# Kernel optimization log

Hardware: AMD Instinct MI355X
Metric: run time of the kernel (lower is better)

Reference implementation:

```python
import jax, jax.numpy as jnp
import numpy as np

B, S, HID, NH, HD, NL = 2, 4096, 1024, 16, 64, 128
N_ITER = 6


def setup_inputs() -> dict:
    key = jax.random.key(0)
    ks = jax.random.split(key, 9)
    s = 0.02
    D = NH * HD
    return {
        "X": jax.random.normal(ks[0], (B, S, HID), jnp.float32),
        "mask": jnp.ones((B, S), jnp.float32),
        "Wq": jax.random.normal(ks[1], (HID, D), jnp.float32) * s,
        "bq": jnp.zeros((D,), jnp.float32),
        "Wk": jax.random.normal(ks[2], (HID, D), jnp.float32) * s,
        "bk": jnp.zeros((D,), jnp.float32),
        "Wv": jax.random.normal(ks[3], (HID, D), jnp.float32) * s,
        "bv": jnp.zeros((D,), jnp.float32),
        "Wo": jax.random.normal(ks[4], (D, HID), jnp.float32) * s,
        "bo": jnp.zeros((HID,), jnp.float32),
    }


def iterative_inv(mat, n_iter=N_ITER):
    # Newton-Schulz style pseudo-inverse iteration (Nystromformer 'original' init)
    I = jnp.eye(mat.shape[-1], dtype=mat.dtype)
    K = mat
    V = K.swapaxes(-1, -2) / jnp.max(jnp.sum(K, axis=-2))
    for _ in range(n_iter):
        KV = K @ V
        V = 0.25 * V @ (13.0 * I - KV @ (15.0 * I - KV @ (7.0 * I - KV)))
    return V


def nystrom_core(Q, K, V, mask):
    # Q,K,V: [B,NH,S,HD], mask: [B,S]
    scale = 1.0 / np.sqrt(np.sqrt(HD))  # 1/d^(1/4) applied to both Q and K
    m = mask[:, None, :, None]
    Q = Q * m * scale
    K = K * m * scale
    seg = S // NL
    # landmarks: mean over contiguous segments -> [B,NH,NL,HD]
    Ql = Q.reshape(B, NH, NL, seg, HD).mean(axis=-2)
    Kl = K.reshape(B, NH, NL, seg, HD).mean(axis=-2)
    k1 = jax.nn.softmax(jnp.einsum('bhsd,bhld->bhsl', Q, Kl), axis=-1)   # [B,NH,S,NL]
    k2 = jax.nn.softmax(jnp.einsum('bhld,bhmd->bhlm', Ql, Kl), axis=-1)  # [B,NH,NL,NL]
    k3 = jax.nn.softmax(
        jnp.einsum('bhld,bhsd->bhls', Ql, K) - 1e9 * (1.0 - mask[:, None, None, :]),
        axis=-1)                                                          # [B,NH,NL,S]
    return k1 @ iterative_inv(k2) @ (k3 @ V)                              # [B,NH,S,HD]


def reference(X, mask, Wq, bq, Wk, bk, Wv, bv, Wo, bo):
    def split(Y):  # [B,S,NH*HD] -> [B,NH,S,HD]
        return Y.reshape(B, S, NH, HD).transpose(0, 2, 1, 3)
    Q = split(X @ Wq + bq)
    K = split(X @ Wk + bk)
    V = split(X @ Wv + bv)
    attn = nystrom_core(Q.astype(jnp.float32), K.astype(jnp.float32),
                        V.astype(jnp.float32), mask.astype(jnp.float32))
    out = attn.transpose(0, 2, 1, 3).reshape(B, S, NH * HD)
    return out @ Wo + bo
```

## Files before the change

### kernel.cpp

```cpp
#include <hip/hip_runtime.h>
#include <math.h>

constexpr int cB = 2, cS = 4096, cHID = 1024, cNH = 16, cHD = 64, cNL = 128, cSEG = 32, cD = 1024, cBH = 32;
constexpr float cSCALE = 0.35355339059327373f;

typedef _Float16 f16x8 __attribute__((ext_vector_type(8)));
typedef float f32x4 __attribute__((ext_vector_type(4)));

__device__ inline void gload_lds16(const void* g, void* l) {
    __builtin_amdgcn_global_load_lds(
        (const __attribute__((address_space(1))) void*)g,
        (__attribute__((address_space(3))) void*)l, 16, 0, 0);
}

__global__ __launch_bounds__(256) void cast_x(const float* __restrict__ X, _Float16* __restrict__ Xh)
{
    int i = (blockIdx.x * 256 + threadIdx.x) * 4;
    float4 v = *reinterpret_cast<const float4*>(X + i);
    union { _Float16 h[4]; ushort4 u; } p;
    p.h[0] = (_Float16)v.x; p.h[1] = (_Float16)v.y; p.h[2] = (_Float16)v.z; p.h[3] = (_Float16)v.w;
    *reinterpret_cast<ushort4*>(Xh + i) = p.u;
}

__global__ __launch_bounds__(256) void wcast_t(
    const float* __restrict__ Wq, const float* __restrict__ Wk,
    const float* __restrict__ Wv, const float* __restrict__ Wo,
    _Float16* __restrict__ WqT, _Float16* __restrict__ WkT,
    _Float16* __restrict__ WvT, _Float16* __restrict__ WoT)
{
    __shared__ float tile[32][33];
    const int wsel = blockIdx.z;
    const float* W = (wsel == 0) ? Wq : (wsel == 1 ? Wk : (wsel == 2 ? Wv : Wo));
    _Float16* WT   = (wsel == 0) ? WqT : (wsel == 1 ? WkT : (wsel == 2 ? WvT : WoT));
    const int n0 = blockIdx.x * 32, k0 = blockIdx.y * 32;
    const int t = threadIdx.x;
    const int r = t >> 3, c = (t & 7) * 4;
    float4 v = *reinterpret_cast<const float4*>(W + (size_t)(k0 + r) * cD + n0 + c);
    tile[r][c] = v.x; tile[r][c + 1] = v.y; tile[r][c + 2] = v.z; tile[r][c + 3] = v.w;
    __syncthreads();
    union { _Float16 h[4]; ushort4 u; } p;
    p.h[0] = (_Float16)tile[c + 0][r]; p.h[1] = (_Float16)tile[c + 1][r];
    p.h[2] = (_Float16)tile[c + 2][r]; p.h[3] = (_Float16)tile[c + 3][r];
    *reinterpret_cast<ushort4*>(WT + (size_t)(n0 + r) * cHID + k0 + c) = p.u;
}

__global__ __launch_bounds__(256) void xm_kernel(
    const float* __restrict__ X, const float* __restrict__ mask,
    float* __restrict__ Xm, float* __restrict__ mbar)
{
    const int bl = blockIdx.x;
    const int b = bl >> 7, l = bl & 127;
    const int c = threadIdx.x * 4;
    float4 a = {0.f, 0.f, 0.f, 0.f};
    float msum = 0.f;
    for (int j = 0; j < cSEG; ++j) {
        float m = mask[b * cS + l * cSEG + j];
        float4 x = *reinterpret_cast<const float4*>(X + ((size_t)(b * cS + l * cSEG + j)) * cHID + c);
        a.x += m * x.x; a.y += m * x.y; a.z += m * x.z; a.w += m * x.w;
        msum += m;
    }
    const float inv = 1.0f / cSEG;
    a.x *= inv; a.y *= inv; a.z *= inv; a.w *= inv;
    *reinterpret_cast<float4*>(Xm + (size_t)bl * cHID + c) = a;
    if (threadIdx.x == 0) mbar[bl] = msum * inv;
}

__global__ __launch_bounds__(256) void qkv_gemm_f16(
    const _Float16* __restrict__ Xh, const float* __restrict__ mask,
    const _Float16* __restrict__ WqT, const _Float16* __restrict__ WkT, const _Float16* __restrict__ WvT,
    const float* __restrict__ bq, const float* __restrict__ bk, const float* __restrict__ bv,
    _Float16* __restrict__ Qh, _Float16* __restrict__ Kh, _Float16* __restrict__ Vh)
{
    __shared__ __align__(16) _Float16 As[128 * 64];
    __shared__ __align__(16) _Float16 Bs[128 * 64];
    const int wsel = blockIdx.z;
    const _Float16* WT = (wsel == 0) ? WqT : (wsel == 1 ? WkT : WvT);
    const float* bias  = (wsel == 0) ? bq  : (wsel == 1 ? bk  : bv);
    _Float16* Y        = (wsel == 0) ? Qh  : (wsel == 1 ? Kh  : Vh);
    const int n0 = blockIdx.x * 128, m0 = blockIdx.y * 128;
    const int t = threadIdx.x;
    const int wave = t >> 6, lane = t & 63;
    const int wm = (wave >> 1) * 64, wn = (wave & 1) * 64;
    const int quad = lane >> 4, l15 = lane & 15;
    const int srow = wave * 8 + (lane >> 3);
    const int scol = (lane & 7) * 8;

    f32x4 acc[4][4];
#pragma unroll
    for (int i = 0; i < 4; ++i)
#pragma unroll
        for (int j = 0; j < 4; ++j) acc[i][j] = (f32x4){0.f, 0.f, 0.f, 0.f};

    for (int k0 = 0; k0 < cHID; k0 += 64) {
        const _Float16* aSrc = Xh + (size_t)(m0 + srow) * cHID + k0 + scol;
        const _Float16* bSrc = WT + (size_t)(n0 + srow) * cHID + k0 + scol;
#pragma unroll
        for (int i = 0; i < 4; ++i) {
            gload_lds16(aSrc + (size_t)(i * 32) * cHID, &As[(wave * 8 + i * 32) * 64]);
            gload_lds16(bSrc + (size_t)(i * 32) * cHID, &Bs[(wave * 8 + i * 32) * 64]);
        }
        __syncthreads();
        f16x8 af[2][4], bf[2][4];
#pragma unroll
        for (int kh = 0; kh < 2; ++kh) {
#pragma unroll
            for (int mt = 0; mt < 4; ++mt)
                af[kh][mt] = *reinterpret_cast<const f16x8*>(&As[(wm + mt * 16 + l15) * 64 + kh * 32 + quad * 8]);
#pragma unroll
            for (int nt = 0; nt < 4; ++nt)
                bf[kh][nt] = *reinterpret_cast<const f16x8*>(&Bs[(wn + nt * 16 + l15) * 64 + kh * 32 + quad * 8]);
        }
#pragma unroll
        for (int kh = 0; kh < 2; ++kh)
#pragma unroll
            for (int mt = 0; mt < 4; ++mt)
#pragma unroll
                for (int nt = 0; nt < 4; ++nt)
                    acc[mt][nt] = __builtin_amdgcn_mfma_f32_16x16x32_f16(af[kh][mt], bf[kh][nt], acc[mt][nt], 0, 0, 0);
        __syncthreads();
    }
#pragma unroll
    for (int mt = 0; mt < 4; ++mt) {
#pragma unroll
        for (int r = 0; r < 4; ++r) {
            int R = m0 + wm + mt * 16 + quad * 4 + r;
            int b = R >> 12, s = R & (cS - 1);
            float msc = (wsel < 2) ? mask[b * cS + s] * cSCALE : 1.0f;
#pragma unroll
            for (int nt = 0; nt < 4; ++nt) {
                int Cc = n0 + wn + nt * 16 + l15;
                int h = Cc >> 6, d = Cc & 63;
                float val = (acc[mt][nt][r] + bias[Cc]) * msc;
                Y[((size_t)(b * cNH + h) * cS + s) * cHD + d] = (_Float16)val;
            }
        }
    }
}

__global__ __launch_bounds__(256) void out_gemm_f16(
    const _Float16* __restrict__ Ah, const _Float16* __restrict__ WT,
    const float* __restrict__ bias, float* __restrict__ Y)
{
    __shared__ __align__(16) _Float16 As[128 * 64];
    __shared__ __align__(16) _Float16 Bs[128 * 64];
    const int n0 = blockIdx.x * 128, m0 = blockIdx.y * 128;
    const int t = threadIdx.x;
    const int wave = t >> 6, lane = t & 63;
    const int wm = (wave >> 1) * 64, wn = (wave & 1) * 64;
    const int quad = lane >> 4, l15 = lane & 15;
    const int srow = wave * 8 + (lane >> 3);
    const int scol = (lane & 7) * 8;

    f32x4 acc[4][4];
#pragma unroll
    for (int i = 0; i < 4; ++i)
#pragma unroll
        for (int j = 0; j < 4; ++j) acc[i][j] = (f32x4){0.f, 0.f, 0.f, 0.f};

    for (int k0 = 0; k0 < cD; k0 += 64) {
        const _Float16* aSrc = Ah + (size_t)(m0 + srow) * cD + k0 + scol;
        const _Float16* bSrc = WT + (size_t)(n0 + srow) * cD + k0 + scol;
#pragma unroll
        for (int i = 0; i < 4; ++i) {
            gload_lds16(aSrc + (size_t)(i * 32) * cD, &As[(wave * 8 + i * 32) * 64]);
            gload_lds16(bSrc + (size_t)(i * 32) * cD, &Bs[(wave * 8 + i * 32) * 64]);
        }
        __syncthreads();
        f16x8 af[2][4], bf[2][4];
#pragma unroll
        for (int kh = 0; kh < 2; ++kh) {
#pragma unroll
            for (int mt = 0; mt < 4; ++mt)
                af[kh][mt] = *reinterpret_cast<const f16x8*>(&As[(wm + mt * 16 + l15) * 64 + kh * 32 + quad * 8]);
#pragma unroll
            for (int nt = 0; nt < 4; ++nt)
                bf[kh][nt] = *reinterpret_cast<const f16x8*>(&Bs[(wn + nt * 16 + l15) * 64 + kh * 32 + quad * 8]);
        }
#pragma unroll
        for (int kh = 0; kh < 2; ++kh)
#pragma unroll
            for (int mt = 0; mt < 4; ++mt)
#pragma unroll
                for (int nt = 0; nt < 4; ++nt)
                    acc[mt][nt] = __builtin_amdgcn_mfma_f32_16x16x32_f16(af[kh][mt], bf[kh][nt], acc[mt][nt], 0, 0, 0);
        __syncthreads();
    }
#pragma unroll
    for (int mt = 0; mt < 4; ++mt) {
#pragma unroll
        for (int r = 0; r < 4; ++r) {
            int R = m0 + wm + mt * 16 + quad * 4 + r;
#pragma unroll
            for (int nt = 0; nt < 4; ++nt) {
                int Cc = n0 + wn + nt * 16 + l15;
                Y[(size_t)R * cHID + Cc] = acc[mt][nt][r] + bias[Cc];
            }
        }
    }
}

__global__ __launch_bounds__(256) void lgemm(
    const float* __restrict__ Xm, const float* __restrict__ mbar,
    const float* __restrict__ Wq, const float* __restrict__ bq,
    const float* __restrict__ Wk, const float* __restrict__ bk,
    float* __restrict__ Ql, float* __restrict__ Kl,
    _Float16* __restrict__ Qlh, _Float16* __restrict__ Klh)
{
    __shared__ __align__(16) float As[16][68];
    __shared__ __align__(16) float Bs[16][68];
    const int tid = threadIdx.x;
    const int wsel = blockIdx.z;
    const float* W    = wsel ? Wk : Wq;
    const float* bias = wsel ? bk : bq;
    float* Yl         = wsel ? Kl : Ql;
    _Float16* Ylh     = wsel ? Klh : Qlh;
    const int c0 = blockIdx.x * 64, r0 = blockIdx.y * 64;
    const int tx = tid & 15, ty = tid >> 4;
    const int am = tid >> 2, ak = (tid & 3) * 4;
    const int bkk = tid >> 4, bn = (tid & 15) * 4;

    float acc[4][4] = {};
    for (int k0 = 0; k0 < cHID; k0 += 16) {
        float4 a4 = *reinterpret_cast<const float4*>(Xm + (size_t)(r0 + am) * cHID + k0 + ak);
        As[ak + 0][am] = a4.x; As[ak + 1][am] = a4.y; As[ak + 2][am] = a4.z; As[ak + 3][am] = a4.w;
        float4 b4 = *reinterpret_cast<const float4*>(W + (size_t)(k0 + bkk) * cD + c0 + bn);
        *reinterpret_cast<float4*>(&Bs[bkk][bn]) = b4;
        __syncthreads();
#pragma unroll
        for (int kk = 0; kk < 16; ++kk) {
            float4 av  = *reinterpret_cast<const float4*>(&As[kk][ty * 4]);
            float4 bv4 = *reinterpret_cast<const float4*>(&Bs[kk][tx * 4]);
            float a_[4] = {av.x, av.y, av.z, av.w};
            float b_[4] = {bv4.x, bv4.y, bv4.z, bv4.w};
#pragma unroll
            for (int i = 0; i < 4; ++i)
#pragma unroll
                for (int j = 0; j < 4; ++j) acc[i][j] += a_[i] * b_[j];
        }
        __syncthreads();
    }
#pragma unroll
    for (int i = 0; i < 4; ++i) {
        int r = r0 + ty * 4 + i;
        int b = r >> 7, l = r & 127;
        float mb = mbar[r];
#pragma unroll
        for (int j = 0; j < 4; ++j) {
            int c = c0 + tx * 4 + j;
            int h = c >> 6, d = c & 63;
            float val = (acc[i][j] + mb * bias[c]) * cSCALE;
            size_t idx = ((size_t)(b * cNH + h) * cNL + l) * cHD + d;
            Yl[idx] = val;
            Ylh[idx] = (_Float16)val;
        }
    }
}

__global__ __launch_bounds__(128) void k2_softmax(
    const float* __restrict__ Ql, const float* __restrict__ Kl, float* __restrict__ k2)
{
    __shared__ __align__(16) float qrow[64];
    __shared__ float red[128];
    int bh = blockIdx.x >> 7, i = blockIdx.x & 127;
    int j = threadIdx.x;
    if (j < 64) qrow[j] = Ql[(bh * cNL + i) * cHD + j];
    __syncthreads();
    const float4* q4  = reinterpret_cast<const float4*>(qrow);
    const float4* kl4 = reinterpret_cast<const float4*>(Kl + (bh * cNL + j) * cHD);
    float dot = 0.f;
#pragma unroll
    for (int u = 0; u < 16; ++u) {
        float4 a = q4[u], b = kl4[u];
        dot += a.x * b.x + a.y * b.y + a.z * b.z + a.w * b.w;
    }
    red[j] = dot; __syncthreads();
    for (int off = 64; off > 0; off >>= 1) { if (j < off) red[j] = fmaxf(red[j], red[j + off]); __syncthreads(); }
    float m = red[0]; __syncthreads();
    float e = expf(dot - m);
    red[j] = e; __syncthreads();
    for (int off = 64; off > 0; off >>= 1) { if (j < off) red[j] += red[j + off]; __syncthreads(); }
    k2[(bh * cNL + i) * cNL + j] = e / red[0];
}

__global__ __launch_bounds__(128) void colsum_max(const float* __restrict__ k2, int* __restrict__ cmax)
{
    __shared__ float red[128];
    int bh = blockIdx.x, j = threadIdx.x;
    float s = 0.f;
    for (int i = 0; i < cNL; ++i) s += k2[(bh * cNL + i) * cNL + j];
    red[j] = s; __syncthreads();
    for (int off = 64; off > 0; off >>= 1) { if (j < off) red[j] = fmaxf(red[j], red[j + off]); __syncthreads(); }
    if (j == 0) atomicMax(cmax, __float_as_int(red[0]));
}

__device__ inline void split2(float v, _Float16& h, _Float16& l) {
    h = (_Float16)v;
    l = (_Float16)(v - (float)h);
}

#define NYS_MFMA(a, b, c) __builtin_amdgcn_mfma_f32_16x16x32_f16((a), (b), (c), 0, 0, 0)

#define NYS_PRODUCT(PH, PL, LH, LL)                                                     \
    {                                                                                   \
        _Pragma("unroll")                                                               \
        for (int nt_ = 0; nt_ < 4; ++nt_) {                                             \
            f32x4 a0_ = (f32x4){0.f, 0.f, 0.f, 0.f};                                    \
            f32x4 a1_ = (f32x4){0.f, 0.f, 0.f, 0.f};                                    \
            _Pragma("unroll")                                                           \
            for (int k0_ = 0; k0_ < 4; ++k0_) {                                         \
                const int boff_ = (wcb + nt_ * 16) * 136 + k0_ * 32 + quad * 8;         \
                f16x8 bh_ = *reinterpret_cast<const f16x8*>(&PH[boff_]);                \
                f16x8 bl_ = *reinterpret_cast<const f16x8*>(&PL[boff_]);                \
                a0_ = NYS_MFMA(LH[0][k0_], bh_, a0_);                                   \
                a1_ = NYS_MFMA(LH[1][k0_], bh_, a1_);                                   \
                a0_ = NYS_MFMA(LL[0][k0_], bh_, a0_);                                   \
                a1_ = NYS_MFMA(LL[1][k0_], bh_, a1_);                                   \
                a0_ = NYS_MFMA(LH[0][k0_], bl_, a0_);                                   \
                a1_ = NYS_MFMA(LH[1][k0_], bl_, a1_);                                   \
            }                                                                           \
            acc[0][nt_] = a0_; acc[1][nt_] = a1_;                                       \
        }                                                                               \
    }

#define NYS_SCATTER_W(alphav)                                                           \
    {                                                                                   \
        _Pragma("unroll")                                                               \
        for (int mt_ = 0; mt_ < 2; ++mt_) {                                             \
            _Pragma("unroll")                                                           \
            for (int nt_ = 0; nt_ < 4; ++nt_) {                                         \
                int col_ = wcb + nt_ * 16;                                              \
                int rb_  = wr * 32 + mt_ * 16 + quad * 4;                               \
                ushort4 ph_, pl_;                                                       \
                _Pragma("unroll")                                                       \
                for (int r_ = 0; r_ < 4; ++r_) {                                        \
                    float v_ = ((rb_ + r_) == col_ ? (alphav) : 0.f) - acc[mt_][nt_][r_]; \
                    _Float16 h_, l_; split2(v_, h_, l_);                                \
                    ((unsigned short*)&ph_)[r_] = __builtin_bit_cast(unsigned short, h_); \
                    ((unsigned short*)&pl_)[r_] = __builtin_bit_cast(unsigned short, l_); \
                }                                                                       \
                *reinterpret_cast<ushort4*>(&Whi_s[col_ * 136 + rb_]) = ph_;            \
                *reinterpret_cast<ushort4*>(&Wlo_s[col_ * 136 + rb_]) = pl_;            \
            }                                                                           \
        }                                                                               \
    }

__global__ __launch_bounds__(512, 2) void nys_fused(
    const float* __restrict__ k2, const int* __restrict__ cmax, float* __restrict__ V6)
{
    __shared__ __align__(16) _Float16 Vhi_s[128 * 136];
    __shared__ __align__(16) _Float16 Vlo_s[128 * 136];
    __shared__ __align__(16) _Float16 Whi_s[128 * 136];
    __shared__ __align__(16) _Float16 Wlo_s[128 * 136];
    const int bh = blockIdx.x;
    const int t = threadIdx.x;
    const int wave = t >> 6, lane = t & 63;
    const int wr = wave >> 1, wc = wave & 1;
    const int quad = lane >> 4, l15 = lane & 15;
    const int wcb = wc * 64 + l15;
    const float* Kg = k2 + (size_t)bh * (cNL * cNL);
    const float invc = 1.0f / __int_as_float(*cmax);

#pragma unroll
    for (int i = 0; i < 8; ++i) {
        int idx = t + i * 512;
        int row = idx >> 5, c4 = (idx & 31) * 4;
        float4 v = *reinterpret_cast<const float4*>(Kg + (size_t)row * cNL + c4);
        ushort4 ph, pl;
        _Float16 h, l;
        split2(v.x * invc, h, l); ((unsigned short*)&ph)[0] = __builtin_bit_cast(unsigned short, h); ((unsigned short*)&pl)[0] = __builtin_bit_cast(unsigned short, l);
        split2(v.y * invc, h, l); ((unsigned short*)&ph)[1] = __builtin_bit_cast(unsigned short, h); ((unsigned short*)&pl)[1] = __builtin_bit_cast(unsigned short, l);
        split2(v.z * invc, h, l); ((unsigned short*)&ph)[2] = __builtin_bit_cast(unsigned short, h); ((unsigned short*)&pl)[2] = __builtin_bit_cast(unsigned short, l);
        split2(v.w * invc, h, l); ((unsigned short*)&ph)[3] = __builtin_bit_cast(unsigned short, h); ((unsigned short*)&pl)[3] = __builtin_bit_cast(unsigned short, l);
        *reinterpret_cast<ushort4*>(&Vhi_s[row * 136 + c4]) = ph;
        *reinterpret_cast<ushort4*>(&Vlo_s[row * 136 + c4]) = pl;
    }

    f16x8 Khi[2][4], Klo[2][4];
#pragma unroll
    for (int mt = 0; mt < 2; ++mt) {
        const int rowL = wr * 32 + mt * 16 + l15;
#pragma unroll
        for (int k0 = 0; k0 < 4; ++k0) {
            const float* src = Kg + (size_t)rowL * cNL + k0 * 32 + quad * 8;
            float4 v0 = *reinterpret_cast<const float4*>(src);
            float4 v1 = *reinterpret_cast<const float4*>(src + 4);
            union { f16x8 v; _Float16 e[8]; } hh, ll;
            split2(v0.x, hh.e[0], ll.e[0]); split2(v0.y, hh.e[1], ll.e[1]);
            split2(v0.z, hh.e[2], ll.e[2]); split2(v0.w, hh.e[3], ll.e[3]);
            split2(v1.x, hh.e[4], ll.e[4]); split2(v1.y, hh.e[5], ll.e[5]);
            split2(v1.z, hh.e[6], ll.e[6]); split2(v1.w, hh.e[7], ll.e[7]);
            Khi[mt][k0] = hh.v; Klo[mt][k0] = ll.v;
        }
    }
    __syncthreads();

    f32x4 acc[2][4];
    f16x8 Ahi[2][4], Alo[2][4];

    for (int it = 0; it < 6; ++it) {
        NYS_PRODUCT(Vhi_s, Vlo_s, Khi, Klo);
        NYS_SCATTER_W(7.0f);
        __syncthreads();

#pragma unroll
        for (int mt = 0; mt < 2; ++mt) {
            const int rowL = wr * 32 + mt * 16 + l15;
#pragma unroll
            for (int k0 = 0; k0 < 4; ++k0) {
                union { f16x8 v; _Float16 e[8]; } hh, ll;
#pragma unroll
                for (int j = 0; j < 8; ++j) {
                    int kk = k0 * 32 + quad * 8 + j;
                    float s = (float)Whi_s[kk * 136 + rowL] + (float)Wlo_s[kk * 136 + rowL];
                    float a = ((kk == rowL) ? 7.0f : 0.0f) - s;
                    split2(a, hh.e[j], ll.e[j]);
                }
                Ahi[mt][k0] = hh.v; Alo[mt][k0] = ll.v;
            }
        }

        NYS_PRODUCT(Whi_s, Wlo_s, Ahi, Alo);
        __syncthreads();
        NYS_SCATTER_W(15.0f);
        __syncthreads();

        NYS_PRODUCT(Whi_s, Wlo_s, Ahi, Alo);
        __syncthreads();
        NYS_SCATTER_W(13.0f);
        __syncthreads();

#pragma unroll
        for (int mt = 0; mt < 2; ++mt)
#pragma unroll
            for (int nt = 0; nt < 4; ++nt) acc[mt][nt] = (f32x4){0.f, 0.f, 0.f, 0.f};
#pragma unroll
        for (int k0 = 0; k0 < 4; ++k0) {
            f16x8 Vlh[2], Vll[2];
#pragma unroll
            for (int mt = 0; mt < 2; ++mt) {
                const int rowL = wr * 32 + mt * 16 + l15;
                union { f16x8 v; _Float16 e[8]; } hh, ll;
#pragma unroll
                for (int j = 0; j < 8; ++j) {
                    int kk = k0 * 32 + quad * 8 + j;
                    hh.e[j] = Vhi_s[kk * 136 + rowL];
                    ll.e[j] = Vlo_s[kk * 136 + rowL];
                }
                Vlh[mt] = hh.v; Vll[mt] = ll.v;
            }
#pragma unroll
            for (int nt = 0; nt < 4; ++nt) {
                const int boff = (wcb + nt * 16) * 136 + k0 * 32 + quad * 8;
                f16x8 bh_ = *reinterpret_cast<const f16x8*>(&Whi_s[boff]);
                f16x8 bl_ = *reinterpret_cast<const f16x8*>(&Wlo_s[boff]);
                acc[0][nt] = NYS_MFMA(Vlh[0], bh_, acc[0][nt]);
                acc[1][nt] = NYS_MFMA(Vlh[1], bh_, acc[1][nt]);
                acc[0][nt] = NYS_MFMA(Vll[0], bh_, acc[0][nt]);
                acc[1][nt] = NYS_MFMA(Vll[1], bh_, acc[1][nt]);
                acc[0][nt] = NYS_MFMA(Vlh[0], bl_, acc[0][nt]);
                acc[1][nt] = NYS_MFMA(Vlh[1], bl_, acc[1][nt]);
            }
        }
        if (it < 5) {
            __syncthreads();
#pragma unroll
            for (int mt = 0; mt < 2; ++mt) {
#pragma unroll
                for (int nt = 0; nt < 4; ++nt) {
                    int col = wcb + nt * 16;
                    int rb  = wr * 32 + mt * 16 + quad * 4;
                    ushort4 ph, pl;
#pragma unroll
                    for (int r = 0; r < 4; ++r) {
                        _Float16 h, l; split2(0.25f * acc[mt][nt][r], h, l);
                        ((unsigned short*)&ph)[r] = __builtin_bit_cast(unsigned short, h);
                        ((unsigned short*)&pl)[r] = __builtin_bit_cast(unsigned short, l);
                    }
                    *reinterpret_cast<ushort4*>(&Vhi_s[col * 136 + rb]) = ph;
                    *reinterpret_cast<ushort4*>(&Vlo_s[col * 136 + rb]) = pl;
                }
            }
            __syncthreads();
        }
    }
#pragma unroll
    for (int mt = 0; mt < 2; ++mt)
#pragma unroll
        for (int nt = 0; nt < 4; ++nt)
#pragma unroll
            for (int r = 0; r < 4; ++r) {
                int row = wr * 32 + mt * 16 + quad * 4 + r;
                int col = wcb + nt * 16;
                V6[(size_t)bh * (cNL * cNL) + row * cNL + col] = 0.25f * acc[mt][nt][r];
            }
}

__global__ __launch_bounds__(256) void vtrans(const _Float16* __restrict__ Vh, _Float16* __restrict__ VTh)
{
    __shared__ ushort T[64][72];
    const int s0 = blockIdx.x * 64, bh = blockIdx.y;
    const int t = threadIdx.x;
    const _Float16* vb = Vh + ((size_t)bh * cS + s0) * cHD;
#pragma unroll
    for (int i = 0; i < 2; ++i) {
        int idx = t + i * 256;
        int row = idx >> 3, c8 = idx & 7;
        f16x8 v = *reinterpret_cast<const f16x8*>(vb + (size_t)row * cHD + c8 * 8);
#pragma unroll
        for (int j = 0; j < 8; ++j) T[row][c8 * 8 + j] = ((ushort*)&v)[j];
    }
    __syncthreads();
    _Float16* vt = VTh + (size_t)bh * cHD * cS;
#pragma unroll
    for (int i = 0; i < 2; ++i) {
        int idx = t + i * 256;
        int d = idx >> 3, s8 = idx & 7;
        f16x8 o;
#pragma unroll
        for (int j = 0; j < 8; ++j) ((ushort*)&o)[j] = T[s8 * 8 + j][d];
        *reinterpret_cast<f16x8*>(vt + (size_t)d * cS + s0 + s8 * 8) = o;
    }
}

__global__ __launch_bounds__(256) void k3v_mfma(
    const _Float16* __restrict__ Qlh, const _Float16* __restrict__ Kh,
    const _Float16* __restrict__ VTh, const float* __restrict__ mask,
    float* __restrict__ Opart, float* __restrict__ mpart, float* __restrict__ spart)
{
    __shared__ __align__(16) _Float16 Ps[128 * 72];
    __shared__ float msk[256];
    const int z = blockIdx.x, bh = blockIdx.y;
    const int b = bh >> 4;
    const int sbase = z * 256;
    const int t = threadIdx.x;
    const int wave = t >> 6, lane = t & 63;
    const int quad = lane >> 4, l15 = lane & 15;

    msk[t] = mask[b * cS + sbase + t];

    f16x8 aq[2][2];
    const _Float16* qlg = Qlh + (size_t)bh * cNL * cHD;
#pragma unroll
    for (int mt = 0; mt < 2; ++mt)
#pragma unroll
        for (int k0 = 0; k0 < 2; ++k0)
            aq[mt][k0] = *reinterpret_cast<const f16x8*>(
                qlg + (size_t)(wave * 32 + mt * 16 + l15) * cHD + k0 * 32 + quad * 8);

    float mrun[2][4], srun[2][4];
    f32x4 accO[2][4];
#pragma unroll
    for (int mt = 0; mt < 2; ++mt)
#pragma unroll
        for (int r = 0; r < 4; ++r) { mrun[mt][r] = -1e30f; srun[mt][r] = 0.f; }
#pragma unroll
    for (int mt = 0; mt < 2; ++mt)
#pragma unroll
        for (int dt = 0; dt < 4; ++dt) accO[mt][dt] = (f32x4){0.f, 0.f, 0.f, 0.f};

    __syncthreads();

    const _Float16* kg = Kh + (size_t)bh * cS * cHD;
    const _Float16* vg = VTh + (size_t)bh * cHD * cS;

    for (int step = 0; step < 4; ++step) {
        const int st = sbase + step * 64;
        f32x4 accS[2][4];
#pragma unroll
        for (int mt = 0; mt < 2; ++mt)
#pragma unroll
            for (int nt = 0; nt < 4; ++nt) accS[mt][nt] = (f32x4){0.f, 0.f, 0.f, 0.f};
#pragma unroll
        for (int k0 = 0; k0 < 2; ++k0)
#pragma unroll
            for (int nt = 0; nt < 4; ++nt) {
                f16x8 bk = *reinterpret_cast<const f16x8*>(
                    kg + (size_t)(st + nt * 16 + l15) * cHD + k0 * 32 + quad * 8);
#pragma unroll
                for (int mt = 0; mt < 2; ++mt)
                    accS[mt][nt] = __builtin_amdgcn_mfma_f32_16x16x32_f16(aq[mt][k0], bk, accS[mt][nt], 0, 0, 0);
            }
#pragma unroll
        for (int nt = 0; nt < 4; ++nt) {
            float pen = 1e9f * (1.0f - msk[step * 64 + nt * 16 + l15]);
#pragma unroll
            for (int mt = 0; mt < 2; ++mt)
#pragma unroll
                for (int r = 0; r < 4; ++r) accS[mt][nt][r] -= pen;
        }
#pragma unroll
        for (int mt = 0; mt < 2; ++mt) {
#pragma unroll
            for (int r = 0; r < 4; ++r) {
                float tmax = fmaxf(fmaxf(accS[mt][0][r], accS[mt][1][r]),
                                   fmaxf(accS[mt][2][r], accS[mt][3][r]));
#pragma unroll
                for (int w = 1; w < 16; w <<= 1) tmax = fmaxf(tmax, __shfl_xor(tmax, w, 16));
                float mnew = fmaxf(mrun[mt][r], tmax);
                float alpha = __expf(mrun[mt][r] - mnew);
                float ts = 0.f;
#pragma unroll
                for (int nt = 0; nt < 4; ++nt) {
                    float e = __expf(accS[mt][nt][r] - mnew);
                    accS[mt][nt][r] = e; ts += e;
                }
#pragma unroll
                for (int w = 1; w < 16; w <<= 1) ts += __shfl_xor(ts, w, 16);
                srun[mt][r] = srun[mt][r] * alpha + ts;
                mrun[mt][r] = mnew;
#pragma unroll
                for (int dt = 0; dt < 4; ++dt) accO[mt][dt][r] *= alpha;
            }
        }
#pragma unroll
        for (int mt = 0; mt < 2; ++mt)
#pragma unroll
            for (int nt = 0; nt < 4; ++nt)
#pragma unroll
                for (int r = 0; r < 4; ++r)
                    Ps[(wave * 32 + mt * 16 + quad * 4 + r) * 72 + nt * 16 + l15] =
                        (_Float16)accS[mt][nt][r];
#pragma unroll
        for (int k0 = 0; k0 < 2; ++k0) {
            f16x8 ap[2];
#pragma unroll
            for (int mt = 0; mt < 2; ++mt)
                ap[mt] = *reinterpret_cast<const f16x8*>(
                    &Ps[(wave * 32 + mt * 16 + l15) * 72 + k0 * 32 + quad * 8]);
#pragma unroll
            for (int dt = 0; dt < 4; ++dt) {
                f16x8 bv = *reinterpret_cast<const f16x8*>(
                    vg + (size_t)(dt * 16 + l15) * cS + st + k0 * 32 + quad * 8);
#pragma unroll
                for (int mt = 0; mt < 2; ++mt)
                    accO[mt][dt] = __builtin_amdgcn_mfma_f32_16x16x32_f16(ap[mt], bv, accO[mt][dt], 0, 0, 0);
            }
        }
    }
    const int rowbase = bh * cNL + wave * 32;
#pragma unroll
    for (int mt = 0; mt < 2; ++mt)
#pragma unroll
        for (int dt = 0; dt < 4; ++dt)
#pragma unroll
            for (int r = 0; r < 4; ++r)
                Opart[(size_t)(z * 4096 + rowbase + mt * 16 + quad * 4 + r) * cHD + dt * 16 + l15] =
                    accO[mt][dt][r];
    if (l15 == 0) {
#pragma unroll
        for (int mt = 0; mt < 2; ++mt)
#pragma unroll
            for (int r = 0; r < 4; ++r) {
                int prow = z * 4096 + rowbase + mt * 16 + quad * 4 + r;
                mpart[prow] = mrun[mt][r];
                spart[prow] = srun[mt][r];
            }
    }
}

__global__ __launch_bounds__(256) void k3v_reduce(
    const float* __restrict__ Opart, const float* __restrict__ mpart,
    const float* __restrict__ spart, float* __restrict__ CV)
{
    const int t = threadIdx.x;
    const int row = blockIdx.x * 4 + (t >> 6);
    const int d = t & 63;
    float mstar = -1e30f;
#pragma unroll
    for (int z = 0; z < 16; ++z) mstar = fmaxf(mstar, mpart[z * 4096 + row]);
    float ssum = 0.f, acc = 0.f;
#pragma unroll
    for (int z = 0; z < 16; ++z) {
        float w = __expf(mpart[z * 4096 + row] - mstar);
        ssum += w * spart[z * 4096 + row];
        acc  += w * Opart[(size_t)(z * 4096 + row) * cHD + d];
    }
    CV[(size_t)row * cHD + d] = acc / ssum;
}

__global__ __launch_bounds__(256) void w2_matmul(
    const float* __restrict__ V6, const float* __restrict__ CV, _Float16* __restrict__ W2T)
{
    __shared__ __align__(16) float CVs[128][64];
    const int bh = blockIdx.x, t = threadIdx.x;
    for (int k = 0; k < 32; ++k) { int idx = t + k * 256; CVs[idx >> 6][idx & 63] = CV[bh * 8192 + idx]; }
    __syncthreads();
    const int tx = t & 15, ty = t >> 4;
    float acc[8][4] = {};
    for (int k = 0; k < 128; ++k) {
        float4 b4 = *reinterpret_cast<const float4*>(&CVs[k][tx * 4]);
#pragma unroll
        for (int i = 0; i < 8; ++i) {
            float a = V6[(bh * cNL + ty * 8 + i) * cNL + k];
            acc[i][0] += a * b4.x; acc[i][1] += a * b4.y; acc[i][2] += a * b4.z; acc[i][3] += a * b4.w;
        }
    }
    _Float16* wt = W2T + (size_t)bh * cHD * cNL;
#pragma unroll
    for (int i = 0; i < 8; ++i)
#pragma unroll
        for (int j = 0; j < 4; ++j)
            wt[(size_t)(tx * 4 + j) * cNL + ty * 8 + i] = (_Float16)acc[i][j];
}

__global__ __launch_bounds__(256) void k1_mfma(
    const _Float16* __restrict__ Qh, const _Float16* __restrict__ Klh,
    const _Float16* __restrict__ W2T, _Float16* __restrict__ ctxh)
{
    __shared__ __align__(16) _Float16 Qs[64 * 72];
    __shared__ __align__(16) _Float16 Ps[64 * 136];
    const int s0 = blockIdx.x * 64, bh = blockIdx.y;
    const int b = bh >> 4, h = bh & 15;
    const int t = threadIdx.x;
    const int wave = t >> 6, lane = t & 63;
    const int quad = lane >> 4, l15 = lane & 15;

    {
        const _Float16* qg = Qh + ((size_t)bh * cS + s0) * cHD;
#pragma unroll
        for (int i = 0; i < 2; ++i) {
            int idx = t + i * 256;
            int row = idx >> 3, c8 = idx & 7;
            *reinterpret_cast<f16x8*>(&Qs[row * 72 + c8 * 8]) =
                *reinterpret_cast<const f16x8*>(qg + (size_t)row * cHD + c8 * 8);
        }
    }
    __syncthreads();

    const _Float16* klg = Klh + (size_t)bh * cNL * cHD;
    f32x4 accS[8];
#pragma unroll
    for (int nt = 0; nt < 8; ++nt) accS[nt] = (f32x4){0.f, 0.f, 0.f, 0.f};
#pragma unroll
    for (int k0 = 0; k0 < 2; ++k0) {
        f16x8 aq = *reinterpret_cast<const f16x8*>(&Qs[(wave * 16 + l15) * 72 + k0 * 32 + quad * 8]);
#pragma unroll
        for (int nt = 0; nt < 8; ++nt) {
            f16x8 bk = *reinterpret_cast<const f16x8*>(klg + (size_t)(nt * 16 + l15) * cHD + k0 * 32 + quad * 8);
            accS[nt] = __builtin_amdgcn_mfma_f32_16x16x32_f16(aq, bk, accS[nt], 0, 0, 0);
        }
    }

    float rmax[4] = {-1e30f, -1e30f, -1e30f, -1e30f};
#pragma unroll
    for (int nt = 0; nt < 8; ++nt)
#pragma unroll
        for (int r = 0; r < 4; ++r) rmax[r] = fmaxf(rmax[r], accS[nt][r]);
#pragma unroll
    for (int r = 0; r < 4; ++r)
#pragma unroll
        for (int w = 1; w < 16; w <<= 1) rmax[r] = fmaxf(rmax[r], __shfl_xor(rmax[r], w, 16));
    float rsum[4] = {0.f, 0.f, 0.f, 0.f};
#pragma unroll
    for (int nt = 0; nt < 8; ++nt)
#pragma unroll
        for (int r = 0; r < 4; ++r) { accS[nt][r] = __expf(accS[nt][r] - rmax[r]); rsum[r] += accS[nt][r]; }
#pragma unroll
    for (int r = 0; r < 4; ++r) {
#pragma unroll
        for (int w = 1; w < 16; w <<= 1) rsum[r] += __shfl_xor(rsum[r], w, 16);
        rsum[r] = 1.0f / rsum[r];
    }
#pragma unroll
    for (int nt = 0; nt < 8; ++nt)
#pragma unroll
        for (int r = 0; r < 4; ++r)
            Ps[(wave * 16 + quad * 4 + r) * 136 + nt * 16 + l15] = (_Float16)(accS[nt][r] * rsum[r]);
    __syncthreads();

    const _Float16* wtg = W2T + (size_t)bh * cHD * cNL;
    f32x4 accO[4];
#pragma unroll
    for (int nt = 0; nt < 4; ++nt) accO[nt] = (f32x4){0.f, 0.f, 0.f, 0.f};
#pragma unroll
    for (int k0 = 0; k0 < 4; ++k0) {
        f16x8 ap = *reinterpret_cast<const f16x8*>(&Ps[(wave * 16 + l15) * 136 + k0 * 32 + quad * 8]);
#pragma unroll
        for (int nt = 0; nt < 4; ++nt) {
            f16x8 bw = *reinterpret_cast<const f16x8*>(wtg + (size_t)(nt * 16 + l15) * cNL + k0 * 32 + quad * 8);
            accO[nt] = __builtin_amdgcn_mfma_f32_16x16x32_f16(ap, bw, accO[nt], 0, 0, 0);
        }
    }
#pragma unroll
    for (int nt = 0; nt < 4; ++nt)
#pragma unroll
        for (int r = 0; r < 4; ++r) {
            int s = s0 + wave * 16 + quad * 4 + r;
            int d = nt * 16 + l15;
            ctxh[((size_t)(b * cS) + s) * cD + h * cHD + d] = (_Float16)accO[nt][r];
        }
}

extern "C" void kernel_launch(void* const* d_in, const int* in_sizes, int n_in,
                              void* d_out, int out_size, void* d_ws, size_t ws_size,
                              hipStream_t stream)
{
    const float* X    = (const float*)d_in[0];
    const float* mask = (const float*)d_in[1];
    const float* Wq   = (const float*)d_in[2];
    const float* bq   = (const float*)d_in[3];
    const float* Wk   = (const float*)d_in[4];
    const float* bk   = (const float*)d_in[5];
    const float* Wv   = (const float*)d_in[6];
    const float* bv   = (const float*)d_in[7];
    const float* Wo   = (const float*)d_in[8];
    const float* bo   = (const float*)d_in[9];
    float* out = (float*)d_out;

    float* ws = (float*)d_ws;
    size_t off = 0;
    const size_t szQKV = (size_t)cBH * cS * cHD;
    const size_t szL   = (size_t)cBH * cNL * cHD;
    const size_t szM   = (size_t)cBH * cNL * cNL;
    float* Qr   = ws + off; off += szQKV;
    float* Kr   = ws + off; off += szQKV;
    float* Vr   = ws + off; off += szQKV;
    _Float16* Xh  = (_Float16*)(ws + off); off += szQKV / 2;
    _Float16* WqT = (_Float16*)(ws + off); off += 524288;
    _Float16* WkT = (_Float16*)(ws + off); off += 524288;
    _Float16* WvT = (_Float16*)(ws + off); off += 524288;
    _Float16* WoT = (_Float16*)(ws + off); off += 524288;
    float* Xm   = ws + off; off += (size_t)cB * cNL * cHID;
    float* mbar = ws + off; off += 256;
    float* Ql  = ws + off; off += szL;
    float* Kl  = ws + off; off += szL;
    float* k2  = ws + off; off += szM;
    float* Vb0 = ws + off; off += szM;
    float* Vb1 = ws + off; off += szM;
    float* Zb  = ws + off; off += szM;
    float* T2b = ws + off; off += szM;
    float* T3b = ws + off; off += szM;
    float* CV  = ws + off; off += szL;
    _Float16* Qlh  = (_Float16*)(ws + off); off += szL / 2;
    _Float16* Klh  = (_Float16*)(ws + off); off += szL / 2;
    _Float16* W2Th = (_Float16*)(ws + off); off += szL / 2;
    int*   cmax = (int*)(ws + off); off += 16;
    float* mpart = ws + off; off += 65536;
    float* spart = ws + off; off += 65536;

    _Float16* Qh   = (_Float16*)Qr;
    float*    Opart = Qr + szQKV / 2;
    _Float16* Kh   = (_Float16*)Kr;
    _Float16* ctxh = (_Float16*)(Kr + szQKV / 2);
    _Float16* Vh   = (_Float16*)Vr;
    _Float16* VTh  = (_Float16*)(Vr + szQKV / 2);

    (void)Vb1; (void)Zb; (void)T2b; (void)T3b;

    hipMemsetAsync(cmax, 0, sizeof(int), stream);

    cast_x<<<(int)(szQKV / 1024), 256, 0, stream>>>(X, Xh);
    wcast_t<<<dim3(32, 32, 4), 256, 0, stream>>>(Wq, Wk, Wv, Wo, WqT, WkT, WvT, WoT);
    xm_kernel<<<cB * cNL, 256, 0, stream>>>(X, mask, Xm, mbar);

    qkv_gemm_f16<<<dim3(cD / 128, (cB * cS) / 128, 3), 256, 0, stream>>>(
        Xh, mask, WqT, WkT, WvT, bq, bk, bv, Qh, Kh, Vh);
    vtrans<<<dim3(cS / 64, cBH), 256, 0, stream>>>(Vh, VTh);
    lgemm<<<dim3(cD / 64, (cB * cNL) / 64, 2), 256, 0, stream>>>(Xm, mbar, Wq, bq, Wk, bk, Ql, Kl, Qlh, Klh);

    k2_softmax<<<cBH * cNL, 128, 0, stream>>>(Ql, Kl, k2);
    colsum_max<<<cBH, 128, 0, stream>>>(k2, cmax);

    nys_fused<<<cBH, 512, 0, stream>>>(k2, cmax, Vb0);

    k3v_mfma<<<dim3(16, cBH), 256, 0, stream>>>(Qlh, Kh, VTh, mask, Opart, mpart, spart);
    k3v_reduce<<<1024, 256, 0, stream>>>(Opart, mpart, spart, CV);
    w2_matmul<<<cBH, 256, 0, stream>>>(Vb0, CV, W2Th);
    k1_mfma<<<dim3(cS / 64, cBH), 256, 0, stream>>>(Qh, Klh, W2Th, ctxh);
    out_gemm_f16<<<dim3(cHID / 128, (cB * cS) / 128), 256, 0, stream>>>(ctxh, WoT, bo, out);
}
```

Measured before the change: 544.3 us.

## Reformulate Newton-Schulz inverse iteration around symmetric K·K^T products

Rewrites the Nyström pseudo-inverse kernel so each iteration works on A = c·K·K^T and a polynomial in it, instead of forming K·V and chaining products with V. The product of per-iteration factors M is accumulated in global ping-pong buffers, and the final multiply by K^T and the 1/c scale move into w2_matmul. The goal is fewer dependent 128x128 matmul stages and LDS transposes per iteration. The cost is extra global traffic for M, a second matmul in w2_matmul, and numerical behaviour that depends on the algebraic identity and on hi/lo fp16 splitting.

```diff
diff --git a/kernel.cpp b/kernel.cpp
--- a/kernel.cpp
+++ b/kernel.cpp
@@ -297,8 +297,22 @@
     h = (_Float16)v;
     l = (_Float16)(v - (float)h);
 }
+__device__ inline unsigned short f16bits(_Float16 h) { return __builtin_bit_cast(unsigned short, h); }
 
 #define NYS_MFMA(a, b, c) __builtin_amdgcn_mfma_f32_16x16x32_f16((a), (b), (c), 0, 0, 0)
+
+#define NYS_PRELOAD(PH, PL, LH, LL)                                                     \
+    {                                                                                   \
+        _Pragma("unroll")                                                               \
+        for (int mt_ = 0; mt_ < 2; ++mt_) {                                             \
+            const int rowL_ = wr * 32 + mt_ * 16 + l15;                                 \
+            _Pragma("unroll")                                                           \
+            for (int k0_ = 0; k0_ < 4; ++k0_) {                                         \
+                LH[mt_][k0_] = *reinterpret_cast<const f16x8*>(&PH[rowL_ * 136 + k0_ * 32 + quad * 8]); \
+                LL[mt_][k0_] = *reinterpret_cast<const f16x8*>(&PL[rowL_ * 136 + k0_ * 32 + quad * 8]); \
+            }                                                                           \
+        }                                                                               \
+    }
 
 #define NYS_PRODUCT(PH, PL, LH, LL)                                                     \
     {                                                                                   \
@@ -322,33 +336,12 @@
         }                                                                               \
     }
 
-#define NYS_SCATTER_W(alphav)                                                           \
-    {                                                                                   \
-        _Pragma("unroll")                                                               \
-        for (int mt_ = 0; mt_ < 2; ++mt_) {                                             \
-            _Pragma("unroll")                                                           \
-            for (int nt_ = 0; nt_ < 4; ++nt_) {                                         \
-                int col_ = wcb + nt_ * 16;                                              \
-                int rb_  = wr * 32 + mt_ * 16 + quad * 4;                               \
-                ushort4 ph_, pl_;                                                       \
-                _Pragma("unroll")                                                       \
-                for (int r_ = 0; r_ < 4; ++r_) {                                        \
-                    float v_ = ((rb_ + r_) == col_ ? (alphav) : 0.f) - acc[mt_][nt_][r_]; \
-                    _Float16 h_, l_; split2(v_, h_, l_);                                \
-                    ((unsigned short*)&ph_)[r_] = __builtin_bit_cast(unsigned short, h_); \
-                    ((unsigned short*)&pl_)[r_] = __builtin_bit_cast(unsigned short, l_); \
-                }                                                                       \
-                *reinterpret_cast<ushort4*>(&Whi_s[col_ * 136 + rb_]) = ph_;            \
-                *reinterpret_cast<ushort4*>(&Wlo_s[col_ * 136 + rb_]) = pl_;            \
-            }                                                                           \
-        }                                                                               \
-    }
-
 __global__ __launch_bounds__(512, 2) void nys_fused(
-    const float* __restrict__ k2, const int* __restrict__ cmax, float* __restrict__ V6)
-{
-    __shared__ __align__(16) _Float16 Vhi_s[128 * 136];
-    __shared__ __align__(16) _Float16 Vlo_s[128 * 136];
+    const float* __restrict__ k2, const int* __restrict__ cmax,
+    float* __restrict__ Mg0, float* __restrict__ Mg1)
+{
+    __shared__ __align__(16) _Float16 Ahi_s[128 * 136];
+    __shared__ __align__(16) _Float16 Alo_s[128 * 136];
     __shared__ __align__(16) _Float16 Whi_s[128 * 136];
     __shared__ __align__(16) _Float16 Wlo_s[128 * 136];
     const int bh = blockIdx.x;
@@ -357,142 +350,153 @@
     const int wr = wave >> 1, wc = wave & 1;
     const int quad = lane >> 4, l15 = lane & 15;
     const int wcb = wc * 64 + l15;
-    const float* Kg = k2 + (size_t)bh * (cNL * cNL);
-    const float invc = 1.0f / __int_as_float(*cmax);
-
-#pragma unroll
-    for (int i = 0; i < 8; ++i) {
-        int idx = t + i * 512;
-        int row = idx >> 5, c4 = (idx & 31) * 4;
-        float4 v = *reinterpret_cast<const float4*>(Kg + (size_t)row * cNL + c4);
-        ushort4 ph, pl;
-        _Float16 h, l;
-        split2(v.x * invc, h, l); ((unsigned short*)&ph)[0] = __builtin_bit_cast(unsigned short, h); ((unsigned short*)&pl)[0] = __builtin_bit_cast(unsigned short, l);
-        split2(v.y * invc, h, l); ((unsigned short*)&ph)[1] = __builtin_bit_cast(unsigned short, h); ((unsigned short*)&pl)[1] = __builtin_bit_cast(unsigned short, l);
-        split2(v.z * invc, h, l); ((unsigned short*)&ph)[2] = __builtin_bit_cast(unsigned short, h); ((unsigned short*)&pl)[2] = __builtin_bit_cast(unsigned short, l);
-        split2(v.w * invc, h, l); ((unsigned short*)&ph)[3] = __builtin_bit_cast(unsigned short, h); ((unsigned short*)&pl)[3] = __builtin_bit_cast(unsigned short, l);
-        *reinterpret_cast<ushort4*>(&Vhi_s[row * 136 + c4]) = ph;
-        *reinterpret_cast<ushort4*>(&Vlo_s[row * 136 + c4]) = pl;
-    }
-
-    f16x8 Khi[2][4], Klo[2][4];
-#pragma unroll
-    for (int mt = 0; mt < 2; ++mt) {
-        const int rowL = wr * 32 + mt * 16 + l15;
-#pragma unroll
-        for (int k0 = 0; k0 < 4; ++k0) {
-            const float* src = Kg + (size_t)rowL * cNL + k0 * 32 + quad * 8;
-            float4 v0 = *reinterpret_cast<const float4*>(src);
-            float4 v1 = *reinterpret_cast<const float4*>(src + 4);
-            union { f16x8 v; _Float16 e[8]; } hh, ll;
-            split2(v0.x, hh.e[0], ll.e[0]); split2(v0.y, hh.e[1], ll.e[1]);
-            split2(v0.z, hh.e[2], ll.e[2]); split2(v0.w, hh.e[3], ll.e[3]);
-            split2(v1.x, hh.e[4], ll.e[4]); split2(v1.y, hh.e[5], ll.e[5]);
-            split2(v1.z, hh.e[6], ll.e[6]); split2(v1.w, hh.e[7], ll.e[7]);
-            Khi[mt][k0] = hh.v; Klo[mt][k0] = ll.v;
+    const float* Kg = k2 + (size_t)bh * 16384;
+    float* Mg0b = Mg0 + (size_t)bh * 16384;
+    float* Mg1b = Mg1 + (size_t)bh * 16384;
+    const float sc = sqrtf(1.0f / __int_as_float(*cmax));
+
+    {
+        const int row = t >> 2, c0 = (t & 3) * 32;
+        const float* src = Kg + row * 128 + c0;
+        _Float16* dh = &Whi_s[row * 136 + c0];
+        _Float16* dl = &Wlo_s[row * 136 + c0];
+#pragma unroll
+        for (int u = 0; u < 32; u += 4) {
+            float4 v = *reinterpret_cast<const float4*>(src + u);
+            ushort4 ph, pl; _Float16 h, l;
+            split2(v.x * sc, h, l); ph.x = f16bits(h); pl.x = f16bits(l);
+            split2(v.y * sc, h, l); ph.y = f16bits(h); pl.y = f16bits(l);
+            split2(v.z * sc, h, l); ph.z = f16bits(h); pl.z = f16bits(l);
+            split2(v.w * sc, h, l); ph.w = f16bits(h); pl.w = f16bits(l);
+            *reinterpret_cast<ushort4*>(dh + u) = ph;
+            *reinterpret_cast<ushort4*>(dl + u) = pl;
         }
     }
     __syncthreads();
 
     f32x4 acc[2][4];
-    f16x8 Ahi[2][4], Alo[2][4];
+    f16x8 Fh[2][4], Fl[2][4];
+
+    NYS_PRELOAD(Whi_s, Wlo_s, Fh, Fl);
+    NYS_PRODUCT(Whi_s, Wlo_s, Fh, Fl);
+#pragma unroll
+    for (int mt = 0; mt < 2; ++mt)
+#pragma unroll
+        for (int nt = 0; nt < 4; ++nt) {
+            const int col = wcb + nt * 16;
+            const int rb  = wr * 32 + mt * 16 + quad * 4;
+            ushort4 ph, pl;
+#pragma unroll
+            for (int r = 0; r < 4; ++r) {
+                _Float16 h, l; split2(acc[mt][nt][r], h, l);
+                ((unsigned short*)&ph)[r] = f16bits(h);
+                ((unsigned short*)&pl)[r] = f16bits(l);
+            }
+            *reinterpret_cast<ushort4*>(&Ahi_s[col * 136 + rb]) = ph;
+            *reinterpret_cast<ushort4*>(&Alo_s[col * 136 + rb]) = pl;
+        }
+    __syncthreads();
 
     for (int it = 0; it < 6; ++it) {
-        NYS_PRODUCT(Vhi_s, Vlo_s, Khi, Klo);
-        NYS_SCATTER_W(7.0f);
-        __syncthreads();
-
-#pragma unroll
-        for (int mt = 0; mt < 2; ++mt) {
-            const int rowL = wr * 32 + mt * 16 + l15;
-#pragma unroll
-            for (int k0 = 0; k0 < 4; ++k0) {
-                union { f16x8 v; _Float16 e[8]; } hh, ll;
-#pragma unroll
-                for (int j = 0; j < 8; ++j) {
-                    int kk = k0 * 32 + quad * 8 + j;
-                    float s = (float)Whi_s[kk * 136 + rowL] + (float)Wlo_s[kk * 136 + rowL];
-                    float a = ((kk == rowL) ? 7.0f : 0.0f) - s;
-                    split2(a, hh.e[j], ll.e[j]);
+        NYS_PRELOAD(Ahi_s, Alo_s, Fh, Fl);
+        NYS_PRODUCT(Ahi_s, Alo_s, Fh, Fl);
+#pragma unroll
+        for (int mt = 0; mt < 2; ++mt)
+#pragma unroll
+            for (int nt = 0; nt < 4; ++nt) {
+                const int col = wcb + nt * 16;
+                const int rb  = wr * 32 + mt * 16 + quad * 4;
+                ushort4 ah = *reinterpret_cast<const ushort4*>(&Ahi_s[col * 136 + rb]);
+                ushort4 al = *reinterpret_cast<const ushort4*>(&Alo_s[col * 136 + rb]);
+                ushort4 ph, pl;
+#pragma unroll
+                for (int r = 0; r < 4; ++r) {
+                    float av = (float)__builtin_bit_cast(_Float16, ((unsigned short*)&ah)[r])
+                             + (float)__builtin_bit_cast(_Float16, ((unsigned short*)&al)[r]);
+                    float v = ((rb + r) == col ? 15.0f : 0.0f) - 7.0f * av + acc[mt][nt][r];
+                    _Float16 h, l; split2(v, h, l);
+                    ((unsigned short*)&ph)[r] = f16bits(h);
+                    ((unsigned short*)&pl)[r] = f16bits(l);
                 }
-                Ahi[mt][k0] = hh.v; Alo[mt][k0] = ll.v;
-            }
-        }
-
-        NYS_PRODUCT(Whi_s, Wlo_s, Ahi, Alo);
-        __syncthreads();
-        NYS_SCATTER_W(15.0f);
-        __syncthreads();
-
-        NYS_PRODUCT(Whi_s, Wlo_s, Ahi, Alo);
-        __syncthreads();
-        NYS_SCATTER_W(13.0f);
-        __syncthreads();
-
+                *reinterpret_cast<ushort4*>(&Whi_s[col * 136 + rb]) = ph;
+                *reinterpret_cast<ushort4*>(&Wlo_s[col * 136 + rb]) = pl;
+            }
+        __syncthreads();
+        NYS_PRODUCT(Whi_s, Wlo_s, Fh, Fl);
+        __syncthreads();
 #pragma unroll
         for (int mt = 0; mt < 2; ++mt)
 #pragma unroll
-            for (int nt = 0; nt < 4; ++nt) acc[mt][nt] = (f32x4){0.f, 0.f, 0.f, 0.f};
-#pragma unroll
-        for (int k0 = 0; k0 < 4; ++k0) {
-            f16x8 Vlh[2], Vll[2];
+            for (int nt = 0; nt < 4; ++nt) {
+                const int col = wcb + nt * 16;
+                const int rb  = wr * 32 + mt * 16 + quad * 4;
+                ushort4 ph, pl; float4 mv;
+#pragma unroll
+                for (int r = 0; r < 4; ++r) {
+                    float v = ((rb + r) == col ? 13.0f : 0.0f) - acc[mt][nt][r];
+                    _Float16 h, l; split2(v, h, l);
+                    ((unsigned short*)&ph)[r] = f16bits(h);
+                    ((unsigned short*)&pl)[r] = f16bits(l);
+                    ((float*)&mv)[r] = 0.25f * v;
+                }
+                *reinterpret_cast<ushort4*>(&Whi_s[col * 136 + rb]) = ph;
+                *reinterpret_cast<ushort4*>(&Wlo_s[col * 136 + rb]) = pl;
+                if (it == 0)
+                    *reinterpret_cast<float4*>(&Mg0b[col * 128 + rb]) = mv;
+            }
+        __syncthreads();
+        NYS_PRODUCT(Whi_s, Wlo_s, Fh, Fl);
+#pragma unroll
+        for (int mt = 0; mt < 2; ++mt)
+#pragma unroll
+            for (int nt = 0; nt < 4; ++nt) {
+                const int col = wcb + nt * 16;
+                const int rb  = wr * 32 + mt * 16 + quad * 4;
+                ushort4 ph, pl;
+#pragma unroll
+                for (int r = 0; r < 4; ++r) {
+                    _Float16 h, l; split2(0.25f * acc[mt][nt][r], h, l);
+                    ((unsigned short*)&ph)[r] = f16bits(h);
+                    ((unsigned short*)&pl)[r] = f16bits(l);
+                }
+                *reinterpret_cast<ushort4*>(&Ahi_s[col * 136 + rb]) = ph;
+                *reinterpret_cast<ushort4*>(&Alo_s[col * 136 + rb]) = pl;
+            }
+        if (it >= 1) {
+            const float* Mr = (it & 1) ? Mg0b : Mg1b;
+            float*       Mw = (it & 1) ? Mg1b : Mg0b;
+            f16x8 Mh[2][4], Ml[2][4];
 #pragma unroll
             for (int mt = 0; mt < 2; ++mt) {
                 const int rowL = wr * 32 + mt * 16 + l15;
-                union { f16x8 v; _Float16 e[8]; } hh, ll;
-#pragma unroll
-                for (int j = 0; j < 8; ++j) {
-                    int kk = k0 * 32 + quad * 8 + j;
-                    hh.e[j] = Vhi_s[kk * 136 + rowL];
-                    ll.e[j] = Vlo_s[kk * 136 + rowL];
+#pragma unroll
+                for (int k0 = 0; k0 < 4; ++k0) {
+                    const float* src = Mr + rowL * 128 + k0 * 32 + quad * 8;
+                    float4 v0 = *reinterpret_cast<const float4*>(src);
+                    float4 v1 = *reinterpret_cast<const float4*>(src + 4);
+                    union { f16x8 v; _Float16 e[8]; } hh, ll;
+                    split2(v0.x, hh.e[0], ll.e[0]); split2(v0.y, hh.e[1], ll.e[1]);
+                    split2(v0.z, hh.e[2], ll.e[2]); split2(v0.w, hh.e[3], ll.e[3]);
+                    split2(v1.x, hh.e[4], ll.e[4]); split2(v1.y, hh.e[5], ll.e[5]);
+                    split2(v1.z, hh.e[6], ll.e[6]); split2(v1.w, hh.e[7], ll.e[7]);
+                    Mh[mt][k0] = hh.v; Ml[mt][k0] = ll.v;
                 }
-                Vlh[mt] = hh.v; Vll[mt] = ll.v;
-            }
-#pragma unroll
-            for (int nt = 0; nt < 4; ++nt) {
-                const int boff = (wcb + nt * 16) * 136 + k0 * 32 + quad * 8;
-                f16x8 bh_ = *reinterpret_cast<const f16x8*>(&Whi_s[boff]);
-                f16x8 bl_ = *reinterpret_cast<const f16x8*>(&Wlo_s[boff]);
-                acc[0][nt] = NYS_MFMA(Vlh[0], bh_, acc[0][nt]);
-                acc[1][nt] = NYS_MFMA(Vlh[1], bh_, acc[1][nt]);
-                acc[0][nt] = NYS_MFMA(Vll[0], bh_, acc[0][nt]);
-                acc[1][nt] = NYS_MFMA(Vll[1], bh_, acc[1][nt]);
-                acc[0][nt] = NYS_MFMA(Vlh[0], bl_, acc[0][nt]);
-                acc[1][nt] = NYS_MFMA(Vlh[1], bl_, acc[1][nt]);
-            }
-        }
-        if (it < 5) {
-            __syncthreads();
-#pragma unroll
-            for (int mt = 0; mt < 2; ++mt) {
+            }
+            NYS_PRODUCT(Whi_s, Wlo_s, Mh, Ml);
+#pragma unroll
+            for (int mt = 0; mt < 2; ++mt)
 #pragma unroll
                 for (int nt = 0; nt < 4; ++nt) {
-                    int col = wcb + nt * 16;
-                    int rb  = wr * 32 + mt * 16 + quad * 4;
-                    ushort4 ph, pl;
-#pragma unroll
-                    for (int r = 0; r < 4; ++r) {
-                        _Float16 h, l; split2(0.25f * acc[mt][nt][r], h, l);
-                        ((unsigned short*)&ph)[r] = __builtin_bit_cast(unsigned short, h);
-                        ((unsigned short*)&pl)[r] = __builtin_bit_cast(unsigned short, l);
-                    }
-                    *reinterpret_cast<ushort4*>(&Vhi_s[col * 136 + rb]) = ph;
-                    *reinterpret_cast<ushort4*>(&Vlo_s[col * 136 + rb]) = pl;
+                    const int col = wcb + nt * 16;
+                    const int rb  = wr * 32 + mt * 16 + quad * 4;
+                    float4 mv;
+#pragma unroll
+                    for (int r = 0; r < 4; ++r) ((float*)&mv)[r] = 0.25f * acc[mt][nt][r];
+                    *reinterpret_cast<float4*>(&Mw[col * 128 + rb]) = mv;
                 }
-            }
-            __syncthreads();
-        }
-    }
-#pragma unroll
-    for (int mt = 0; mt < 2; ++mt)
-#pragma unroll
-        for (int nt = 0; nt < 4; ++nt)
-#pragma unroll
-            for (int r = 0; r < 4; ++r) {
-                int row = wr * 32 + mt * 16 + quad * 4 + r;
-                int col = wcb + nt * 16;
-                V6[(size_t)bh * (cNL * cNL) + row * cNL + col] = 0.25f * acc[mt][nt][r];
-            }
+        }
+        __syncthreads();
+    }
 }
 
 __global__ __launch_bounds__(256) void vtrans(const _Float16* __restrict__ Vh, _Float16* __restrict__ VTh)
@@ -679,28 +683,51 @@
 }
 
 __global__ __launch_bounds__(256) void w2_matmul(
-    const float* __restrict__ V6, const float* __restrict__ CV, _Float16* __restrict__ W2T)
-{
-    __shared__ __align__(16) float CVs[128][64];
+    const float* __restrict__ k2, const float* __restrict__ M6,
+    const int* __restrict__ cmax, const float* __restrict__ CV,
+    _Float16* __restrict__ W2T)
+{
+    __shared__ __align__(16) float CVs[128][68];
+    __shared__ __align__(16) float Us[128][68];
     const int bh = blockIdx.x, t = threadIdx.x;
-    for (int k = 0; k < 32; ++k) { int idx = t + k * 256; CVs[idx >> 6][idx & 63] = CV[bh * 8192 + idx]; }
-    __syncthreads();
-    const int tx = t & 15, ty = t >> 4;
-    float acc[8][4] = {};
-    for (int k = 0; k < 128; ++k) {
-        float4 b4 = *reinterpret_cast<const float4*>(&CVs[k][tx * 4]);
-#pragma unroll
-        for (int i = 0; i < 8; ++i) {
-            float a = V6[(bh * cNL + ty * 8 + i) * cNL + k];
-            acc[i][0] += a * b4.x; acc[i][1] += a * b4.y; acc[i][2] += a * b4.z; acc[i][3] += a * b4.w;
-        }
-    }
-    _Float16* wt = W2T + (size_t)bh * cHD * cNL;
-#pragma unroll
-    for (int i = 0; i < 8; ++i)
-#pragma unroll
-        for (int j = 0; j < 4; ++j)
-            wt[(size_t)(tx * 4 + j) * cNL + ty * 8 + i] = (_Float16)acc[i][j];
+    const float invc = 1.0f / __int_as_float(*cmax);
+    for (int k = 0; k < 32; ++k) { int idx = t + k * 256; CVs[idx >> 6][idx & 63] = CV[(size_t)bh * 8192 + idx]; }
+    __syncthreads();
+    const float* Mg = M6 + (size_t)bh * 16384;
+    {
+        const int tx = t & 15, ty = t >> 4;
+        float acc[8][4] = {};
+        for (int k = 0; k < 128; ++k) {
+            float4 b4 = *reinterpret_cast<const float4*>(&CVs[k][tx * 4]);
+#pragma unroll
+            for (int i = 0; i < 8; ++i) {
+                float a = Mg[(ty * 8 + i) * 128 + k];
+                acc[i][0] += a * b4.x; acc[i][1] += a * b4.y; acc[i][2] += a * b4.z; acc[i][3] += a * b4.w;
+            }
+        }
+#pragma unroll
+        for (int i = 0; i < 8; ++i)
+#pragma unroll
+            for (int j = 0; j < 4; ++j)
+                Us[ty * 8 + i][tx * 4 + j] = acc[i][j];
+    }
+    __syncthreads();
+    {
+        const int l = t & 127, dg = (t >> 7) * 32;
+        float acc2[32];
+#pragma unroll
+        for (int dd = 0; dd < 32; ++dd) acc2[dd] = 0.f;
+        const float* kg = k2 + (size_t)bh * 16384;
+        for (int j = 0; j < 128; ++j) {
+            float kv = kg[j * 128 + l];
+#pragma unroll
+            for (int dd = 0; dd < 32; ++dd) acc2[dd] += kv * Us[j][dg + dd];
+        }
+        _Float16* wt = W2T + (size_t)bh * (cHD * cNL);
+#pragma unroll
+        for (int dd = 0; dd < 32; ++dd)
+            wt[(size_t)(dg + dd) * cNL + l] = (_Float16)(acc2[dd] * invc);
+    }
 }
 
 __global__ __launch_bounds__(256) void k1_mfma(
@@ -825,8 +852,8 @@
     float* Ql  = ws + off; off += szL;
     float* Kl  = ws + off; off += szL;
     float* k2  = ws + off; off += szM;
-    float* Vb0 = ws + off; off += szM;
-    float* Vb1 = ws + off; off += szM;
+    float* Mg0 = ws + off; off += szM;
+    float* Mg1 = ws + off; off += szM;
     float* Zb  = ws + off; off += szM;
     float* T2b = ws + off; off += szM;
     float* T3b = ws + off; off += szM;
@@ -845,7 +872,7 @@
     _Float16* Vh   = (_Float16*)Vr;
     _Float16* VTh  = (_Float16*)(Vr + szQKV / 2);
 
-    (void)Vb1; (void)Zb; (void)T2b; (void)T3b;
+    (void)Zb; (void)T2b; (void)T3b;
 
     hipMemsetAsync(cmax, 0, sizeof(int), stream);
 
@@ -861,11 +888,11 @@
     k2_softmax<<<cBH * cNL, 128, 0, stream>>>(Ql, Kl, k2);
     colsum_max<<<cBH, 128, 0, stream>>>(k2, cmax);
 
-    nys_fused<<<cBH, 512, 0, stream>>>(k2, cmax, Vb0);
+    nys_fused<<<cBH, 512, 0, stream>>>(k2, cmax, Mg0, Mg1);
 
     k3v_mfma<<<dim3(16, cBH), 256, 0, stream>>>(Qlh, Kh, VTh, mask, Opart, mpart, spart);
     k3v_reduce<<<1024, 256, 0, stream>>>(Opart, mpart, spart, CV);
-    w2_matmul<<<cBH, 256, 0, stream>>>(Vb0, CV, W2Th);
+    w2_matmul<<<cBH, 256, 0, stream>>>(k2, Mg1, cmax, CV, W2Th);
     k1_mfma<<<dim3(cS / 64, cBH), 256, 0, stream>>>(Qh, Klh, W2Th, ctxh);
     out_gemm_f16<<<dim3(cHID / 128, (cB * cS) / 128), 256, 0, stream>>>(ctxh, WoT, bo, out);
 }
```

New measurement: 496.1 us. 8.9% less time.
